# Optimization experiments

Hardware: AMD Instinct MI355X
Metric: run time of the kernel (lower is better)

The kernel has to match this reference:

```python
import jax, jax.numpy as jnp
import numpy as np

EPS = 1e-8  # torch F.cosine_similarity default eps


def setup_inputs() -> dict:
    key = jax.random.key(0)
    k1, k2 = jax.random.split(key)
    x = jax.random.normal(k1, (16384, 1024), dtype=jnp.float32)
    label = jax.random.randint(k2, (16384, 64), 0, 2).astype(jnp.int64)
    w = jnp.asarray(10.0, dtype=jnp.float32)  # nn.Parameter init_w
    b = jnp.asarray(-5.0, dtype=jnp.float32)  # nn.Parameter init_b
    return {"x": x, "label": label, "w": w, "b": b}


def reference(x, label, w, b):
    # Append the 'no-label' column for rows whose label vector is all zero.
    extra = (label.sum(axis=1) == 0).astype(label.dtype)[:, None]
    lab = jnp.concatenate([label, extra], axis=1).astype(x.dtype)  # [B, C]

    counts = lab.sum(axis=0)                  # [C] positives per centroid
    active = counts > 0                       # torch drops empty columns; we mask them

    # Centroids: mean of x over rows carrying each label (scatter-mean as GEMM).
    anchor = (lab.T @ x) / jnp.maximum(counts, 1.0)[:, None]   # [C, D]

    # Cosine similarity between every sample and every centroid.
    xn = jnp.maximum(jnp.linalg.norm(x, axis=1), EPS)          # [B]
    an = jnp.maximum(jnp.linalg.norm(anchor, axis=1), EPS)     # [C]
    cos = (x @ anchor.T) / (xn[:, None] * an[None, :])          # [B, C]

    logits = cos * w + b
    # Removing empty columns from softmax == setting their logits to -inf.
    logits = jnp.where(active[None, :], logits, -jnp.inf)
    logp = jax.nn.log_softmax(logits, axis=1)                   # [B, C]

    # Row expansion in torch duplicates sample i once per positive label j;
    # the logits row only depends on i, so CE over expanded rows is a
    # pair-weighted mean of -logp[i, j] over positive (i, j) pairs.
    n_pairs = lab.sum()
    nloss = -jnp.sum(jnp.where(lab > 0, logp, 0.0)) / n_pairs
    return nloss
```

## Files before the change

### kernel.cpp

```cpp
#include <hip/hip_runtime.h>
#include <hip/hip_bf16.h>
#include <stdint.h>

#define NROWS 16384
#define NDIM  1024
#define NLAB  64
#define NC    65
#define CPAD  80

typedef float float4v __attribute__((ext_vector_type(4)));
typedef short short8  __attribute__((ext_vector_type(8)));

static constexpr size_t CNT_B   = 0;
static constexpr size_t ACT_B   = 320;
static constexpr size_t SCALE_B = 352;
static constexpr size_t WSUM_B  = 672;
static constexpr size_t ZERO_BYTES = 676;
static constexpr size_t MASK_B  = 1024;
static constexpr size_t XN2_B   = 132096;
static constexpr size_t LFRAG_B = 197632;
static constexpr size_t BFRAG_B = 2819072;
static constexpr size_t XAF_B   = 2982912;
static constexpr size_t XCOL_B  = 36537344;
static constexpr size_t PART_B  = 70091776;
static constexpr size_t SLAB    = (size_t)CPAD * NDIM * 4;

__device__ __forceinline__ unsigned short bf16u(float f) {
    __hip_bfloat16 h = __float2bfloat16(f);
    return __builtin_bit_cast(unsigned short, h);
}
__device__ __forceinline__ unsigned pk2(float a, float b) {
    return (unsigned)bf16u(a) | ((unsigned)bf16u(b) << 16);
}

__global__ __launch_bounds__(256) void k01_prep(const float* __restrict__ x,
                                                const int* __restrict__ label,
                                                unsigned short* __restrict__ xAfrag,
                                                unsigned short* __restrict__ xcol,
                                                float* __restrict__ xn2g,
                                                unsigned long long* __restrict__ masks,
                                                unsigned* __restrict__ counts,
                                                unsigned short* __restrict__ lfrag) {
    __shared__ unsigned short xt[16][1034];
    __shared__ unsigned cnt[NC];
    __shared__ unsigned long long smask[64];
    int t = threadIdx.x;
    if (blockIdx.x < 1024) {
        int rt = blockIdx.x;
        int r = t >> 4, cpos = t & 15;
        const float* src = x + ((size_t)rt * 16 + r) * NDIM + cpos * 4;
        float sq = 0.f;
#pragma unroll
        for (int i = 0; i < 16; ++i) {
            float4 f = *(const float4*)(src + i * 64);
            sq += f.x * f.x + f.y * f.y + f.z * f.z + f.w * f.w;
            *(uint2*)&xt[r][cpos * 4 + i * 64] = make_uint2(pk2(f.x, f.y), pk2(f.z, f.w));
        }
#pragma unroll
        for (int m = 1; m < 16; m <<= 1) sq += __shfl_xor(sq, m, 16);
        if (cpos == 0) xn2g[rt * 16 + r] = sq;
        __syncthreads();
        {
            int slot = t & 63, wv = t >> 6;
            int q = slot >> 4, col = slot & 15;
#pragma unroll
            for (int s = 0; s < 8; ++s) {
                int kb = s * 4 + wv;
                uint4 v = *(const uint4*)&xt[col][kb * 32 + q * 8];
                ((uint4*)xAfrag)[((size_t)rt * 32 + kb) * 64 + slot] = v;
            }
        }
#pragma unroll
        for (int s = 0; s < 8; ++s) {
            int dim = s * 128 + (t >> 1);
            int rh = (t & 1) * 8;
            unsigned short tmp[8];
#pragma unroll
            for (int j = 0; j < 8; ++j) tmp[j] = xt[rh + j][dim];
            uint4 v;
            v.x = (unsigned)tmp[0] | ((unsigned)tmp[1] << 16);
            v.y = (unsigned)tmp[2] | ((unsigned)tmp[3] << 16);
            v.z = (unsigned)tmp[4] | ((unsigned)tmp[5] << 16);
            v.w = (unsigned)tmp[6] | ((unsigned)tmp[7] << 16);
            ((uint4*)xcol)[(size_t)rt * 2048 + s * 256 + t] = v;
        }
        return;
    }
    int bid = blockIdx.x - 1024;
    if (t < NC) cnt[t] = 0;
    __syncthreads();
    int wave = t >> 6, lane = t & 63;
    int rowblock = bid * 64;
    unsigned creg = 0, zreg = 0;
#pragma unroll 4
    for (int p = 0; p < 16; ++p) {
        int row = rowblock + p * 4 + wave;
        int v = label[row * NLAB + lane];
        unsigned long long m = __ballot(v != 0);
        creg += (unsigned)((m >> lane) & 1ull);
        if (lane == 0) {
            masks[row] = m;
            smask[p * 4 + wave] = m;
            zreg += (m == 0ull) ? 1u : 0u;
        }
    }
    atomicAdd(&cnt[lane], creg);
    if (lane == 0 && zreg) atomicAdd(&cnt[64], zreg);
    __syncthreads();
    if (t < NC) atomicAdd(&counts[t], cnt[t]);
    for (int pid = t; pid < 640; pid += 256) {
        int rt2l = pid / 320, rem = pid % 320;
        int ct = rem >> 6, ln = rem & 63;
        int q = ln >> 4, col = ln & 15;
        int c = ct * 16 + col;
        int rbase = rt2l * 32 + q * 8;
        unsigned pk[4];
#pragma unroll
        for (int jp = 0; jp < 4; ++jp) {
            unsigned long long m0 = smask[rbase + jp * 2], m1 = smask[rbase + jp * 2 + 1];
            unsigned b0, b1;
            if (c < 64)       { b0 = (unsigned)((m0 >> c) & 1ull); b1 = (unsigned)((m1 >> c) & 1ull); }
            else if (c == 64) { b0 = (m0 == 0ull); b1 = (m1 == 0ull); }
            else              { b0 = 0u; b1 = 0u; }
            pk[jp] = (b0 ? 0x3F80u : 0u) | (b1 ? 0x3F800000u : 0u);
        }
        uint4 w = make_uint4(pk[0], pk[1], pk[2], pk[3]);
        ((uint4*)lfrag)[((size_t)(bid * 2 + rt2l) * 5 + ct) * 64 + ln] = w;
    }
}

__global__ __launch_bounds__(256) void k2_sums(const unsigned short* __restrict__ xcol,
                                               const unsigned short* __restrict__ lfrag,
                                               float* __restrict__ partial,
                                               int kslices) {
    int t = threadIdx.x, wave = t >> 6, lane = t & 63;
    int q = lane >> 4, col = lane & 15;
    int dgroup = blockIdx.x & 15, ks = blockIdx.x >> 4;
    int nkb = (NROWS / kslices) >> 5;
    int kb0 = ks * nkb;
    int d = dgroup * 64 + wave * 16 + col;
    const uint4* B = (const uint4*)xcol;
    const uint4* A = (const uint4*)lfrag;
    size_t bidx0 = (size_t)d * 2 + (q & 1);
    int qh = q >> 1;

    float4v acc[5];
#pragma unroll
    for (int ct = 0; ct < 5; ++ct) acc[ct] = (float4v){0.f, 0.f, 0.f, 0.f};

#pragma unroll 4
    for (int i = 0; i < nkb; ++i) {
        int kb = kb0 + i;
        uint4 braw = B[(size_t)(kb * 2 + qh) * 2048 + bidx0];
        short8 bf = __builtin_bit_cast(short8, braw);
#pragma unroll
        for (int ct = 0; ct < 5; ++ct) {
            uint4 araw = A[((size_t)kb * 5 + ct) * 64 + lane];
            short8 af = __builtin_bit_cast(short8, araw);
            acc[ct] = __builtin_amdgcn_mfma_f32_16x16x32_bf16(af, bf, acc[ct], 0, 0, 0);
        }
    }
    float* pb = partial + (size_t)ks * CPAD * NDIM;
#pragma unroll
    for (int ct = 0; ct < 5; ++ct)
#pragma unroll
        for (int reg = 0; reg < 4; ++reg)
            pb[(size_t)(ct * 16 + q * 4 + reg) * NDIM + d] = acc[ct][reg];
}

__global__ __launch_bounds__(256) void k2b_fuse(const float* __restrict__ wptr,
                                                const unsigned* __restrict__ counts,
                                                const float* __restrict__ partial,
                                                int kslices,
                                                unsigned short* __restrict__ bfrag,
                                                float* __restrict__ scale,
                                                unsigned* __restrict__ act) {
    int c = blockIdx.x, t = threadIdx.x;
    int d0 = t * 4;
    const float* p = partial + (size_t)c * NDIM + d0;
    float4 s = make_float4(0.f, 0.f, 0.f, 0.f);
#pragma unroll 8
    for (int sl = 0; sl < kslices; ++sl) {
        float4 v = *(const float4*)(p + (size_t)sl * CPAD * NDIM);
        s.x += v.x; s.y += v.y; s.z += v.z; s.w += v.w;
    }
    unsigned cnt = counts[c];
    float invc = 1.0f / (float)(cnt > 0u ? cnt : 1u);
    float ax = s.x * invc, ay = s.y * invc, az = s.z * invc, aw = s.w * invc;
    float ss = ax * ax + ay * ay + az * az + aw * aw;
    __shared__ float red[8];
#pragma unroll
    for (int m = 32; m >= 1; m >>= 1) ss += __shfl_xor(ss, m, 64);
    if ((t & 63) == 0) red[t >> 6] = ss;
    __syncthreads();
    ss = red[0] + red[1] + red[2] + red[3];

    float denom = fmaxf(sqrtf(ss), 1e-8f);
    float rinv = invc / denom;
    unsigned short h0 = bf16u(s.x * rinv), h1 = bf16u(s.y * rinv);
    unsigned short h2 = bf16u(s.z * rinv), h3 = bf16u(s.w * rinv);
    int ct = c >> 4, colc = c & 15;
    int kb = d0 >> 5, q = (d0 >> 3) & 3, j0 = d0 & 7;
    size_t sidx = ((((size_t)ct * 32 + kb) * 64) + q * 16 + colc) * 8 + j0;
    *(uint2*)(bfrag + sidx) =
        make_uint2(((unsigned)h1 << 16) | h0, ((unsigned)h3 << 16) | h2);

    float f0 = __bfloat162float(__builtin_bit_cast(__hip_bfloat16, h0));
    float f1 = __bfloat162float(__builtin_bit_cast(__hip_bfloat16, h1));
    float f2 = __bfloat162float(__builtin_bit_cast(__hip_bfloat16, h2));
    float f3 = __bfloat162float(__builtin_bit_cast(__hip_bfloat16, h3));
    float nb2 = f0 * f0 + f1 * f1 + f2 * f2 + f3 * f3;
#pragma unroll
    for (int m = 32; m >= 1; m >>= 1) nb2 += __shfl_xor(nb2, m, 64);
    if ((t & 63) == 0) red[4 + (t >> 6)] = nb2;
    __syncthreads();
    if (t == 0) {
        float n2 = red[4] + red[5] + red[6] + red[7];
        scale[c] = (n2 > 0.f) ? (wptr[0] / sqrtf(n2)) : 0.f;
        if (cnt > 0u) atomicOr(&act[c >> 4], 1u << (c & 15));
    }
}

__global__ __launch_bounds__(256, 4) void k3_loss(const unsigned short* __restrict__ xAfrag,
                                                  const unsigned short* __restrict__ bfrag,
                                                  const float* __restrict__ xn2g,
                                                  const unsigned long long* __restrict__ masks,
                                                  const unsigned* __restrict__ act,
                                                  const float* __restrict__ scale,
                                                  const float* __restrict__ bptr,
                                                  float* __restrict__ wsum) {
    __shared__ float xch[3][64 * 20];
    int t = threadIdx.x, kh = t >> 6, lane = t & 63;
    int q = lane >> 4, col = lane & 15;
    int rt = blockIdx.x;
    int rowbase = rt * 16;
    const uint4* A = (const uint4*)xAfrag;
    const uint4* B = (const uint4*)bfrag;

    float4v acc[5];
#pragma unroll
    for (int ct = 0; ct < 5; ++ct) acc[ct] = (float4v){0.f, 0.f, 0.f, 0.f};

#pragma unroll
    for (int s = 0; s < 8; ++s) {
        int kb = kh * 8 + s;
        uint4 araw = A[((size_t)rt * 32 + kb) * 64 + lane];
        short8 af = __builtin_bit_cast(short8, araw);
#pragma unroll
        for (int ct = 0; ct < 5; ++ct) {
            uint4 braw = B[((size_t)ct * 32 + kb) * 64 + lane];
            short8 bf = __builtin_bit_cast(short8, braw);
            acc[ct] = __builtin_amdgcn_mfma_f32_16x16x32_bf16(af, bf, acc[ct], 0, 0, 0);
        }
    }
    if (kh) {
        float* dst = &xch[kh - 1][lane * 20];
#pragma unroll
        for (int ct = 0; ct < 5; ++ct)
#pragma unroll
            for (int r = 0; r < 4; ++r) dst[ct * 4 + r] = acc[ct][r];
    }
    __syncthreads();
    if (kh) return;
#pragma unroll
    for (int j = 0; j < 3; ++j) {
        const float* src = &xch[j][lane * 20];
#pragma unroll
        for (int ct = 0; ct < 5; ++ct)
#pragma unroll
            for (int r = 0; r < 4; ++r) acc[ct][r] += src[ct * 4 + r];
    }

    float bv = bptr[0];
    float sc[5]; unsigned ab[5];
#pragma unroll
    for (int ct = 0; ct < 5; ++ct) { sc[ct] = scale[ct * 16 + col]; ab[ct] = act[ct]; }

    float contrib = 0.f;
#pragma unroll
    for (int reg = 0; reg < 4; ++reg) {
        int rl = q * 4 + reg;
        int row = rowbase + rl;
        float inv = 1.0f / fmaxf(sqrtf(xn2g[row]), 1e-8f);
        unsigned long long mask = masks[row];
        float v[5]; float lmax = -1e30f;
#pragma unroll
        for (int ct = 0; ct < 5; ++ct) {
            float lg = acc[ct][reg] * sc[ct] * inv + bv;
            bool a = (ab[ct] >> col) & 1u;
            v[ct] = a ? lg : -1e30f;
            lmax = fmaxf(lmax, v[ct]);
        }
#pragma unroll
        for (int m = 1; m < 16; m <<= 1) lmax = fmaxf(lmax, __shfl_xor(lmax, m, 16));
        float es = 0.f;
#pragma unroll
        for (int ct = 0; ct < 5; ++ct) es += expf(v[ct] - lmax);
#pragma unroll
        for (int m = 1; m < 16; m <<= 1) es += __shfl_xor(es, m, 16);
        float lse = lmax + logf(es);
        float ps = 0.f;
#pragma unroll
        for (int ct = 0; ct < 5; ++ct) {
            int c = ct * 16 + col;
            bool pos = (c < 64) ? (((mask >> c) & 1ull) != 0ull)
                                : ((c == 64) ? (mask == 0ull) : false);
            ps += pos ? v[ct] : 0.f;
        }
#pragma unroll
        for (int m = 1; m < 16; m <<= 1) ps += __shfl_xor(ps, m, 16);
        float npos = mask ? (float)__popcll(mask) : 1.0f;
        float crow = ps - npos * lse;
        if (col == 0) contrib += crow;
    }
#pragma unroll
    for (int m = 1; m < 64; m <<= 1) contrib += __shfl_xor(contrib, m, 64);
    if (lane == 0) atomicAdd(wsum, contrib);
}

__global__ void k4_final(const unsigned* __restrict__ counts,
                         const float* __restrict__ wsum,
                         float* __restrict__ out) {
    if (threadIdx.x == 0 && blockIdx.x == 0) {
        float np = 0.f;
        for (int c = 0; c < NC; ++c) np += (float)counts[c];
        out[0] = -wsum[0] / np;
    }
}

extern "C" void kernel_launch(void* const* d_in, const int* in_sizes, int n_in,
                              void* d_out, int out_size, void* d_ws, size_t ws_size,
                              hipStream_t stream) {
    (void)in_sizes; (void)n_in; (void)out_size;
    const float* x = (const float*)d_in[0];
    const int* label = (const int*)d_in[1];
    const float* w = (const float*)d_in[2];
    const float* b = (const float*)d_in[3];

    char* ws = (char*)d_ws;
    unsigned* counts = (unsigned*)(ws + CNT_B);
    unsigned* act = (unsigned*)(ws + ACT_B);
    float* scale = (float*)(ws + SCALE_B);
    float* wsum = (float*)(ws + WSUM_B);
    unsigned long long* masks = (unsigned long long*)(ws + MASK_B);
    float* xn2g = (float*)(ws + XN2_B);
    unsigned short* lfrag = (unsigned short*)(ws + LFRAG_B);
    unsigned short* bfrag = (unsigned short*)(ws + BFRAG_B);
    unsigned short* xAfrag = (unsigned short*)(ws + XAF_B);
    unsigned short* xcol = (unsigned short*)(ws + XCOL_B);
    float* partial = (float*)(ws + PART_B);

    int kslices = 32;
    while (kslices > 8 && PART_B + (size_t)kslices * SLAB > ws_size) kslices >>= 1;

    hipMemsetAsync(d_ws, 0, ZERO_BYTES, stream);
    hipLaunchKernelGGL(k01_prep, dim3(1024 + 256), dim3(256), 0, stream,
                       x, label, xAfrag, xcol, xn2g, masks, counts, lfrag);
    hipLaunchKernelGGL(k2_sums, dim3(16 * kslices), dim3(256), 0, stream,
                       xcol, lfrag, partial, kslices);
    hipLaunchKernelGGL(k2b_fuse, dim3(CPAD), dim3(256), 0, stream,
                       w, counts, partial, kslices, bfrag, scale, act);
    hipLaunchKernelGGL(k3_loss, dim3(NROWS / 16), dim3(256), 0, stream,
                       xAfrag, bfrag, xn2g, masks, act, scale, b, wsum);
    hipLaunchKernelGGL(k4_final, dim3(1), dim3(64), 0, stream, counts, wsum, (float*)d_out);
}
```

Before: 162.3 us.

## Remove memset and final kernel via per-block count partials and last-block finalize

Global atomic counts are replaced with per-block partial count arrays that k2b_fuse reduces, which also resets wsum and a completion counter. That removes the workspace memset. The separate k4_final launch is folded into k3_loss through a last-block-done counter with a threadfence. kslices goes from 32 to 64 and k2_sums gets an occupancy hint. The aim is fewer launches and less atomic contention, at the cost of more partial-sum traffic in k2b_fuse.

```diff
diff --git a/kernel.cpp b/kernel.cpp
--- a/kernel.cpp
+++ b/kernel.cpp
@@ -11,18 +11,19 @@
 typedef float float4v __attribute__((ext_vector_type(4)));
 typedef short short8  __attribute__((ext_vector_type(8)));
 
-static constexpr size_t CNT_B   = 0;
-static constexpr size_t ACT_B   = 320;
-static constexpr size_t SCALE_B = 352;
-static constexpr size_t WSUM_B  = 672;
-static constexpr size_t ZERO_BYTES = 676;
-static constexpr size_t MASK_B  = 1024;
-static constexpr size_t XN2_B   = 132096;
-static constexpr size_t LFRAG_B = 197632;
-static constexpr size_t BFRAG_B = 2819072;
-static constexpr size_t XAF_B   = 2982912;
-static constexpr size_t XCOL_B  = 36537344;
-static constexpr size_t PART_B  = 70091776;
+static constexpr size_t SCALE_B = 0;
+static constexpr size_t ACTB_B  = 320;
+static constexpr size_t WSUM_B  = 400;
+static constexpr size_t CTR_B   = 404;
+static constexpr size_t CNTF_B  = 448;
+static constexpr size_t CNTP_B  = 1024;
+static constexpr size_t MASK_B  = 83968;
+static constexpr size_t XN2_B   = 215040;
+static constexpr size_t LFRAG_B = 280576;
+static constexpr size_t BFRAG_B = 2902016;
+static constexpr size_t XAF_B   = 3065856;
+static constexpr size_t XCOL_B  = 36620288;
+static constexpr size_t PART_B  = 70174720;
 static constexpr size_t SLAB    = (size_t)CPAD * NDIM * 4;
 
 __device__ __forceinline__ unsigned short bf16u(float f) {
@@ -39,7 +40,7 @@
                                                 unsigned short* __restrict__ xcol,
                                                 float* __restrict__ xn2g,
                                                 unsigned long long* __restrict__ masks,
-                                                unsigned* __restrict__ counts,
+                                                unsigned* __restrict__ cntpart,
                                                 unsigned short* __restrict__ lfrag) {
     __shared__ unsigned short xt[16][1034];
     __shared__ unsigned cnt[NC];
@@ -107,7 +108,7 @@
     atomicAdd(&cnt[lane], creg);
     if (lane == 0 && zreg) atomicAdd(&cnt[64], zreg);
     __syncthreads();
-    if (t < NC) atomicAdd(&counts[t], cnt[t]);
+    if (t < 80) cntpart[bid * 80 + t] = (t < NC) ? cnt[t] : 0u;
     for (int pid = t; pid < 640; pid += 256) {
         int rt2l = pid / 320, rem = pid % 320;
         int ct = rem >> 6, ln = rem & 63;
@@ -129,10 +130,10 @@
     }
 }
 
-__global__ __launch_bounds__(256) void k2_sums(const unsigned short* __restrict__ xcol,
-                                               const unsigned short* __restrict__ lfrag,
-                                               float* __restrict__ partial,
-                                               int kslices) {
+__global__ __launch_bounds__(256, 4) void k2_sums(const unsigned short* __restrict__ xcol,
+                                                  const unsigned short* __restrict__ lfrag,
+                                                  float* __restrict__ partial,
+                                                  int kslices) {
     int t = threadIdx.x, wave = t >> 6, lane = t & 63;
     int q = lane >> 4, col = lane & 15;
     int dgroup = blockIdx.x & 15, ks = blockIdx.x >> 4;
@@ -169,13 +170,26 @@
 }
 
 __global__ __launch_bounds__(256) void k2b_fuse(const float* __restrict__ wptr,
-                                                const unsigned* __restrict__ counts,
+                                                const unsigned* __restrict__ cntpart,
                                                 const float* __restrict__ partial,
                                                 int kslices,
                                                 unsigned short* __restrict__ bfrag,
                                                 float* __restrict__ scale,
-                                                unsigned* __restrict__ act) {
+                                                unsigned char* __restrict__ actB,
+                                                unsigned* __restrict__ countsF,
+                                                float* __restrict__ wsum,
+                                                unsigned* __restrict__ counter) {
     int c = blockIdx.x, t = threadIdx.x;
+    __shared__ float red[8];
+    __shared__ unsigned credu[4];
+    if (c == 0 && t == 1) { *wsum = 0.f; *counter = 0u; }
+    unsigned cv = cntpart[t * 80 + c];
+#pragma unroll
+    for (int m = 32; m >= 1; m >>= 1) cv += __shfl_xor(cv, m, 64);
+    if ((t & 63) == 0) credu[t >> 6] = cv;
+    __syncthreads();
+    unsigned cnt = credu[0] + credu[1] + credu[2] + credu[3];
+
     int d0 = t * 4;
     const float* p = partial + (size_t)c * NDIM + d0;
     float4 s = make_float4(0.f, 0.f, 0.f, 0.f);
@@ -184,11 +198,9 @@
         float4 v = *(const float4*)(p + (size_t)sl * CPAD * NDIM);
         s.x += v.x; s.y += v.y; s.z += v.z; s.w += v.w;
     }
-    unsigned cnt = counts[c];
     float invc = 1.0f / (float)(cnt > 0u ? cnt : 1u);
     float ax = s.x * invc, ay = s.y * invc, az = s.z * invc, aw = s.w * invc;
     float ss = ax * ax + ay * ay + az * az + aw * aw;
-    __shared__ float red[8];
 #pragma unroll
     for (int m = 32; m >= 1; m >>= 1) ss += __shfl_xor(ss, m, 64);
     if ((t & 63) == 0) red[t >> 6] = ss;
@@ -217,7 +229,8 @@
     if (t == 0) {
         float n2 = red[4] + red[5] + red[6] + red[7];
         scale[c] = (n2 > 0.f) ? (wptr[0] / sqrtf(n2)) : 0.f;
-        if (cnt > 0u) atomicOr(&act[c >> 4], 1u << (c & 15));
+        actB[c] = (cnt > 0u) ? 1 : 0;
+        countsF[c] = cnt;
     }
 }
 
@@ -225,10 +238,13 @@
                                                   const unsigned short* __restrict__ bfrag,
                                                   const float* __restrict__ xn2g,
                                                   const unsigned long long* __restrict__ masks,
-                                                  const unsigned* __restrict__ act,
+                                                  const unsigned char* __restrict__ actB,
                                                   const float* __restrict__ scale,
+                                                  const unsigned* __restrict__ countsF,
                                                   const float* __restrict__ bptr,
-                                                  float* __restrict__ wsum) {
+                                                  float* __restrict__ wsum,
+                                                  unsigned* __restrict__ counter,
+                                                  float* __restrict__ out) {
     __shared__ float xch[3][64 * 20];
     int t = threadIdx.x, kh = t >> 6, lane = t & 63;
     int q = lane >> 4, col = lane & 15;
@@ -272,9 +288,9 @@
     }
 
     float bv = bptr[0];
-    float sc[5]; unsigned ab[5];
-#pragma unroll
-    for (int ct = 0; ct < 5; ++ct) { sc[ct] = scale[ct * 16 + col]; ab[ct] = act[ct]; }
+    float sc[5]; unsigned char ab[5];
+#pragma unroll
+    for (int ct = 0; ct < 5; ++ct) { sc[ct] = scale[ct * 16 + col]; ab[ct] = actB[ct * 16 + col]; }
 
     float contrib = 0.f;
 #pragma unroll
@@ -287,8 +303,7 @@
 #pragma unroll
         for (int ct = 0; ct < 5; ++ct) {
             float lg = acc[ct][reg] * sc[ct] * inv + bv;
-            bool a = (ab[ct] >> col) & 1u;
-            v[ct] = a ? lg : -1e30f;
+            v[ct] = ab[ct] ? lg : -1e30f;
             lmax = fmaxf(lmax, v[ct]);
         }
 #pragma unroll
@@ -315,16 +330,16 @@
     }
 #pragma unroll
     for (int m = 1; m < 64; m <<= 1) contrib += __shfl_xor(contrib, m, 64);
-    if (lane == 0) atomicAdd(wsum, contrib);
-}
-
-__global__ void k4_final(const unsigned* __restrict__ counts,
-                         const float* __restrict__ wsum,
-                         float* __restrict__ out) {
-    if (threadIdx.x == 0 && blockIdx.x == 0) {
-        float np = 0.f;
-        for (int c = 0; c < NC; ++c) np += (float)counts[c];
-        out[0] = -wsum[0] / np;
+    if (lane == 0) {
+        atomicAdd(wsum, contrib);
+        __threadfence();
+        unsigned old = atomicAdd(counter, 1u);
+        if (old == (unsigned)gridDim.x - 1u) {
+            float np = 0.f;
+            for (int c = 0; c < NC; ++c) np += (float)countsF[c];
+            float tot = atomicAdd(wsum, 0.0f);
+            out[0] = -tot / np;
+        }
     }
 }
 
@@ -338,10 +353,12 @@
     const float* b = (const float*)d_in[3];
 
     char* ws = (char*)d_ws;
-    unsigned* counts = (unsigned*)(ws + CNT_B);
-    unsigned* act = (unsigned*)(ws + ACT_B);
     float* scale = (float*)(ws + SCALE_B);
+    unsigned char* actB = (unsigned char*)(ws + ACTB_B);
     float* wsum = (float*)(ws + WSUM_B);
+    unsigned* counter = (unsigned*)(ws + CTR_B);
+    unsigned* countsF = (unsigned*)(ws + CNTF_B);
+    unsigned* cntpart = (unsigned*)(ws + CNTP_B);
     unsigned long long* masks = (unsigned long long*)(ws + MASK_B);
     float* xn2g = (float*)(ws + XN2_B);
     unsigned short* lfrag = (unsigned short*)(ws + LFRAG_B);
@@ -350,17 +367,16 @@
     unsigned short* xcol = (unsigned short*)(ws + XCOL_B);
     float* partial = (float*)(ws + PART_B);
 
-    int kslices = 32;
+    int kslices = 64;
     while (kslices > 8 && PART_B + (size_t)kslices * SLAB > ws_size) kslices >>= 1;
 
-    hipMemsetAsync(d_ws, 0, ZERO_BYTES, stream);
     hipLaunchKernelGGL(k01_prep, dim3(1024 + 256), dim3(256), 0, stream,
-                       x, label, xAfrag, xcol, xn2g, masks, counts, lfrag);
+                       x, label, xAfrag, xcol, xn2g, masks, cntpart, lfrag);
     hipLaunchKernelGGL(k2_sums, dim3(16 * kslices), dim3(256), 0, stream,
                        xcol, lfrag, partial, kslices);
     hipLaunchKernelGGL(k2b_fuse, dim3(CPAD), dim3(256), 0, stream,
-                       w, counts, partial, kslices, bfrag, scale, act);
+                       w, cntpart, partial, kslices, bfrag, scale, actB, countsF, wsum, counter);
     hipLaunchKernelGGL(k3_loss, dim3(NROWS / 16), dim3(256), 0, stream,
-                       xAfrag, bfrag, xn2g, masks, act, scale, b, wsum);
-    hipLaunchKernelGGL(k4_final, dim3(1), dim3(64), 0, stream, counts, wsum, (float*)d_out);
-}
+                       xAfrag, bfrag, xn2g, masks, actB, scale, countsF, b, wsum, counter,
+                       (float*)d_out);
+}
```

New measurement: 178.5 us. 10.0% more time.
